# Optimization experiments

Measured on AMD Instinct MI355X. Metric: run time of the kernel, lower is better.

## Reference

```python
import jax, jax.numpy as jnp
import numpy as np

RES = 32
EPS = 1e-06


def setup_inputs() -> dict:
    key = jax.random.key(0)
    k1, k2 = jax.random.split(key)
    features = jax.random.normal(k1, (16, 32768, 64), dtype=jnp.float32)
    # coords roughly in [-1, 1] as the docstring assumes
    coords = jax.random.uniform(k2, (16, 32768, 3), dtype=jnp.float32, minval=-1.0, maxval=1.0)
    return {"features": features, "coords": coords}


def reference(features, coords):
    R = RES
    B, N, C = features.shape
    # center and normalize coords to [0, 1]
    centered = coords - coords.mean(axis=1, keepdims=True)               # [B,N,3]
    max_norm = jnp.linalg.norm(centered, axis=2, keepdims=True).max(axis=1, keepdims=True)  # [B,1,1]
    normalized_coords = centered / (max_norm * 2 + EPS) + 0.5            # [B,N,3] in [0,1]
    # voxel indices
    vi = jnp.round(normalized_coords * (R - 1)).astype(jnp.int32)        # [B,N,3]
    idx = vi[..., 0] * (R * R) + vi[..., 1] * R + vi[..., 2]             # [B,N]
    # flatten batch into segment ids: segment = b*R^3 + idx
    flat_idx = (idx + jnp.arange(B, dtype=jnp.int32)[:, None] * (R ** 3)).reshape(-1)  # [B*N]
    sums = jax.ops.segment_sum(features.reshape(B * N, C), flat_idx,
                               num_segments=B * R ** 3).reshape(B, R ** 3, C)
    counts = jax.ops.segment_sum(jnp.ones((B * N,), features.dtype), flat_idx,
                                 num_segments=B * R ** 3).reshape(B, R ** 3, 1)
    avg = sums / jnp.maximum(counts, 1.0)                                 # [B,R^3,C]
    avg_voxel_features = avg.transpose(0, 2, 1).reshape(B, C, R, R, R)
    return avg_voxel_features, normalized_coords
```

## Files before the change

kernel.cpp:

```cpp
#include <hip/hip_runtime.h>

#define NB     16
#define NPTS   32768
#define NC     64
#define RES    32
#define R3     32768
#define EPSV   1e-6f
#define SLICES 8
#define NPT    (NB * NPTS)

#define QSCALE 1048576.0f
#define QINV   (1.0f / 1048576.0f)
#define QBIAS  8388608

__global__ __launch_bounds__(256) void stats_partial_kernel(const float* __restrict__ coords,
                                                            double* __restrict__ psum) {
    const int blk = blockIdx.x;
    const int b = blk >> 3, s = blk & (SLICES - 1);
    const int cnt = NPTS / SLICES;
    const float* cb = coords + ((size_t)b * NPTS + (size_t)s * cnt) * 3;

    double sx = 0.0, sy = 0.0, sz = 0.0;
    for (int n = threadIdx.x; n < cnt; n += 256) {
        sx += (double)cb[n * 3 + 0];
        sy += (double)cb[n * 3 + 1];
        sz += (double)cb[n * 3 + 2];
    }
    __shared__ double sd[256];
    const int t = threadIdx.x;
    sd[t] = sx; __syncthreads();
    for (int o = 128; o > 0; o >>= 1) { if (t < o) sd[t] += sd[t + o]; __syncthreads(); }
    if (t == 0) psum[blk * 3 + 0] = sd[0];
    __syncthreads();
    sd[t] = sy; __syncthreads();
    for (int o = 128; o > 0; o >>= 1) { if (t < o) sd[t] += sd[t + o]; __syncthreads(); }
    if (t == 0) psum[blk * 3 + 1] = sd[0];
    __syncthreads();
    sd[t] = sz; __syncthreads();
    for (int o = 128; o > 0; o >>= 1) { if (t < o) sd[t] += sd[t + o]; __syncthreads(); }
    if (t == 0) psum[blk * 3 + 2] = sd[0];
}

__global__ __launch_bounds__(256) void maxnorm_partial_kernel(const float* __restrict__ coords,
                                                              const double* __restrict__ psum,
                                                              float* __restrict__ pmax) {
    const int blk = blockIdx.x;
    const int b = blk >> 3, s = blk & (SLICES - 1);
    const int cnt = NPTS / SLICES;

    double dx = 0.0, dy = 0.0, dz = 0.0;
    for (int i = 0; i < SLICES; i++) {
        dx += psum[(b * SLICES + i) * 3 + 0];
        dy += psum[(b * SLICES + i) * 3 + 1];
        dz += psum[(b * SLICES + i) * 3 + 2];
    }
    const float mx = (float)(dx / (double)NPTS);
    const float my = (float)(dy / (double)NPTS);
    const float mz = (float)(dz / (double)NPTS);

    const float* cb = coords + ((size_t)b * NPTS + (size_t)s * cnt) * 3;
    float mn = 0.0f;
    for (int n = threadIdx.x; n < cnt; n += 256) {
        float ax = cb[n * 3 + 0] - mx;
        float ay = cb[n * 3 + 1] - my;
        float az = cb[n * 3 + 2] - mz;
        mn = fmaxf(mn, sqrtf(ax * ax + ay * ay + az * az));
    }
    __shared__ float sf[256];
    const int t = threadIdx.x;
    sf[t] = mn; __syncthreads();
    for (int o = 128; o > 0; o >>= 1) { if (t < o) sf[t] = fmaxf(sf[t], sf[t + o]); __syncthreads(); }
    if (t == 0) pmax[blk] = sf[0];
}

__global__ __launch_bounds__(64) void stats_final_kernel(const double* __restrict__ psum,
                                                         const float* __restrict__ pmax,
                                                         float* __restrict__ stats) {
    const int b = threadIdx.x;
    if (b < NB) {
        double dx = 0.0, dy = 0.0, dz = 0.0; float m = 0.0f;
        for (int i = 0; i < SLICES; i++) {
            dx += psum[(b * SLICES + i) * 3 + 0];
            dy += psum[(b * SLICES + i) * 3 + 1];
            dz += psum[(b * SLICES + i) * 3 + 2];
            m  = fmaxf(m, pmax[b * SLICES + i]);
        }
        stats[b * 4 + 0] = (float)(dx / (double)NPTS);
        stats[b * 4 + 1] = (float)(dy / (double)NPTS);
        stats[b * 4 + 2] = (float)(dz / (double)NPTS);
        stats[b * 4 + 3] = m * 2.0f + EPSV;
    }
}

__global__ __launch_bounds__(256) void scatter_packed_kernel(const float* __restrict__ features,
                                                             const float* __restrict__ coords,
                                                             const float* __restrict__ stats,
                                                             unsigned long long* __restrict__ acc,
                                                             float* __restrict__ nc_out,
                                                             unsigned* __restrict__ counts) {
    const int tid = blockIdx.x * 256 + threadIdx.x;
    const int p   = tid >> 5;
    const int h   = tid & 31;
    const int b   = p >> 15;

    const float mx = stats[b * 4 + 0];
    const float my = stats[b * 4 + 1];
    const float mz = stats[b * 4 + 2];
    const float s  = stats[b * 4 + 3];

    const float nx = (coords[(size_t)p * 3 + 0] - mx) / s + 0.5f;
    const float ny = (coords[(size_t)p * 3 + 1] - my) / s + 0.5f;
    const float nz = (coords[(size_t)p * 3 + 2] - mz) / s + 0.5f;

    int vx = (int)rintf(nx * (float)(RES - 1));
    int vy = (int)rintf(ny * (float)(RES - 1));
    int vz = (int)rintf(nz * (float)(RES - 1));
    vx = min(max(vx, 0), RES - 1);
    vy = min(max(vy, 0), RES - 1);
    vz = min(max(vz, 0), RES - 1);
    const int vox = vx * (RES * RES) + vy * RES + vz;

    if (h < 3) {
        const float v = (h == 0) ? nx : ((h == 1) ? ny : nz);
        nc_out[(size_t)p * 3 + h] = v;
    }
    if (h == 0) atomicAdd(&counts[((size_t)b << 15) + vox], 1u);

    const float2 f2 = *(const float2*)(features + ((size_t)p << 6) + (h << 1));
    const int q0 = (int)rintf(f2.x * QSCALE);
    const int q1 = (int)rintf(f2.y * QSCALE);
    const unsigned long long pk =
        (unsigned long long)(unsigned)(q0 + QBIAS) |
        ((unsigned long long)(unsigned)(q1 + QBIAS) << 32);

    atomicAdd(&acc[(((size_t)((b << 15) + vox)) << 5) + h], pk);
}

__global__ __launch_bounds__(256) void finalize_kernel(const unsigned long long* __restrict__ acc,
                                                       const unsigned* __restrict__ counts,
                                                       float* __restrict__ out0) {
    const int bkt = blockIdx.x;
    const int b   = bkt >> 9;
    const int v0  = (bkt & 511) << 6;
    const int tid = threadIdx.x;

    __shared__ float    t[64][65];
    __shared__ float    rcs[64];
    __shared__ unsigned cnts[64];

    unsigned c = 0;
    if (tid < 64) {
        c = counts[((size_t)b << 15) + v0 + tid];
        cnts[tid] = c;
        rcs[tid]  = 1.0f / fmaxf((float)c, 1.0f);
    }
    const int any = __syncthreads_or(c != 0);

    float* o = out0 + ((size_t)b << 21) + v0;
    const int vl0 = (tid & 15) << 2;

    if (!any) {
        const float4 z = {0.0f, 0.0f, 0.0f, 0.0f};
#pragma unroll
        for (int k = 0; k < 4; k++) {
            const int ch = (tid >> 4) + (k << 4);
            *(float4*)(o + ((size_t)ch << 15) + vl0) = z;
        }
        return;
    }

    const unsigned long long* a = acc + (((size_t)((b << 15) + v0)) << 5);
#pragma unroll
    for (int i = 0; i < 8; i++) {
        const int f  = i * 256 + tid;
        const int v  = f >> 5;
        const int hh = f & 31;
        const unsigned long long u = a[f];
        const unsigned cv = cnts[v];
        const long long bias = (long long)cv * (long long)QBIAS;
        const long long q0 = (long long)(u & 0xffffffffull) - bias;
        const long long q1 = (long long)(u >> 32) - bias;
        const float rc = rcs[v] * QINV;
        t[v][2 * hh + 0] = (float)q0 * rc;
        t[v][2 * hh + 1] = (float)q1 * rc;
    }
    __syncthreads();

#pragma unroll
    for (int k = 0; k < 4; k++) {
        const int ch = (tid >> 4) + (k << 4);
        float4 v4;
        v4.x = t[vl0 + 0][ch];
        v4.y = t[vl0 + 1][ch];
        v4.z = t[vl0 + 2][ch];
        v4.w = t[vl0 + 3][ch];
        *(float4*)(o + ((size_t)ch << 15) + vl0) = v4;
    }
}

extern "C" void kernel_launch(void* const* d_in, const int* in_sizes, int n_in,
                              void* d_out, int out_size, void* d_ws, size_t ws_size,
                              hipStream_t stream) {
    const float* features = (const float*)d_in[0];
    const float* coords   = (const float*)d_in[1];

    float* out0   = (float*)d_out;
    float* nc_out = (float*)d_out + (size_t)NB * NC * R3;

    char* ws = (char*)d_ws;
    float*              stats  = (float*)ws;
    double*             psum   = (double*)(ws + 256);
    float*              pmax   = (float*)(ws + 3584);
    unsigned*           counts = (unsigned*)(ws + 4096);
    unsigned long long* acc    = (unsigned long long*)(ws + 4096 + (size_t)NB * R3 * 4);

    const size_t counts_bytes = (size_t)NB * R3 * 4;
    const size_t acc_bytes    = (size_t)NB * R3 * 32 * 8;

    hipMemsetAsync(counts, 0, counts_bytes + acc_bytes, stream);

    stats_partial_kernel<<<NB * SLICES, 256, 0, stream>>>(coords, psum);
    maxnorm_partial_kernel<<<NB * SLICES, 256, 0, stream>>>(coords, psum, pmax);
    stats_final_kernel<<<1, 64, 0, stream>>>(psum, pmax, stats);

    scatter_packed_kernel<<<(NPT * 32) / 256, 256, 0, stream>>>(features, coords, stats,
                                                                acc, nc_out, counts);

    finalize_kernel<<<NB * 512, 256, 0, stream>>>(acc, counts, out0);
}
```

Baseline: 383.3 us.

## Fuse coord stats into one kernel and remap blocks for XCD-local atomics

Three stats kernels (partial sum, partial max-norm, final combine) are merged into a single kernel with one 1024-thread block per batch, removing two launches and the workspace round trips. The scatter and finalize kernels remap blockIdx so that blocks dispatched round-robin to the same XCD handle a contiguous range of points or voxels. This is meant to keep each batch's accumulator atomics and reads within one XCD's L2. The trade-off is that the stats pass now runs on only 16 blocks, so it has less parallelism.

```diff
diff --git a/kernel.cpp b/kernel.cpp
--- a/kernel.cpp
+++ b/kernel.cpp
@@ -6,89 +6,59 @@
 #define RES    32
 #define R3     32768
 #define EPSV   1e-6f
-#define SLICES 8
 #define NPT    (NB * NPTS)
 
 #define QSCALE 1048576.0f
 #define QINV   (1.0f / 1048576.0f)
 #define QBIAS  8388608
 
-__global__ __launch_bounds__(256) void stats_partial_kernel(const float* __restrict__ coords,
-                                                            double* __restrict__ psum) {
-    const int blk = blockIdx.x;
-    const int b = blk >> 3, s = blk & (SLICES - 1);
-    const int cnt = NPTS / SLICES;
-    const float* cb = coords + ((size_t)b * NPTS + (size_t)s * cnt) * 3;
+__global__ __launch_bounds__(1024) void stats_kernel(const float* __restrict__ coords,
+                                                     float* __restrict__ stats) {
+    const int b = blockIdx.x;
+    const int t = threadIdx.x;
+    const float* cb = coords + (size_t)b * NPTS * 3;
 
     double sx = 0.0, sy = 0.0, sz = 0.0;
-    for (int n = threadIdx.x; n < cnt; n += 256) {
+    for (int n = t; n < NPTS; n += 1024) {
         sx += (double)cb[n * 3 + 0];
         sy += (double)cb[n * 3 + 1];
         sz += (double)cb[n * 3 + 2];
     }
-    __shared__ double sd[256];
-    const int t = threadIdx.x;
+
+    __shared__ double sd[1024];
+    __shared__ float  res[3];
+
     sd[t] = sx; __syncthreads();
-    for (int o = 128; o > 0; o >>= 1) { if (t < o) sd[t] += sd[t + o]; __syncthreads(); }
-    if (t == 0) psum[blk * 3 + 0] = sd[0];
+    for (int o = 512; o > 0; o >>= 1) { if (t < o) sd[t] += sd[t + o]; __syncthreads(); }
+    if (t == 0) res[0] = (float)(sd[0] / (double)NPTS);
     __syncthreads();
     sd[t] = sy; __syncthreads();
-    for (int o = 128; o > 0; o >>= 1) { if (t < o) sd[t] += sd[t + o]; __syncthreads(); }
-    if (t == 0) psum[blk * 3 + 1] = sd[0];
+    for (int o = 512; o > 0; o >>= 1) { if (t < o) sd[t] += sd[t + o]; __syncthreads(); }
+    if (t == 0) res[1] = (float)(sd[0] / (double)NPTS);
     __syncthreads();
     sd[t] = sz; __syncthreads();
-    for (int o = 128; o > 0; o >>= 1) { if (t < o) sd[t] += sd[t + o]; __syncthreads(); }
-    if (t == 0) psum[blk * 3 + 2] = sd[0];
-}
+    for (int o = 512; o > 0; o >>= 1) { if (t < o) sd[t] += sd[t + o]; __syncthreads(); }
+    if (t == 0) res[2] = (float)(sd[0] / (double)NPTS);
+    __syncthreads();
 
-__global__ __launch_bounds__(256) void maxnorm_partial_kernel(const float* __restrict__ coords,
-                                                              const double* __restrict__ psum,
-                                                              float* __restrict__ pmax) {
-    const int blk = blockIdx.x;
-    const int b = blk >> 3, s = blk & (SLICES - 1);
-    const int cnt = NPTS / SLICES;
+    const float mx = res[0], my = res[1], mz = res[2];
 
-    double dx = 0.0, dy = 0.0, dz = 0.0;
-    for (int i = 0; i < SLICES; i++) {
-        dx += psum[(b * SLICES + i) * 3 + 0];
-        dy += psum[(b * SLICES + i) * 3 + 1];
-        dz += psum[(b * SLICES + i) * 3 + 2];
+    float mn = 0.0f;
+    for (int n = t; n < NPTS; n += 1024) {
+        float dx = cb[n * 3 + 0] - mx;
+        float dy = cb[n * 3 + 1] - my;
+        float dz = cb[n * 3 + 2] - mz;
+        mn = fmaxf(mn, sqrtf(dx * dx + dy * dy + dz * dz));
     }
-    const float mx = (float)(dx / (double)NPTS);
-    const float my = (float)(dy / (double)NPTS);
-    const float mz = (float)(dz / (double)NPTS);
+    float* sf = (float*)sd;
+    sf[t] = mn; __syncthreads();
+    for (int o = 512; o > 0; o >>= 1) { if (t < o) sf[t] = fmaxf(sf[t], sf[t + o]); __syncthreads(); }
 
-    const float* cb = coords + ((size_t)b * NPTS + (size_t)s * cnt) * 3;
-    float mn = 0.0f;
-    for (int n = threadIdx.x; n < cnt; n += 256) {
-        float ax = cb[n * 3 + 0] - mx;
-        float ay = cb[n * 3 + 1] - my;
-        float az = cb[n * 3 + 2] - mz;
-        mn = fmaxf(mn, sqrtf(ax * ax + ay * ay + az * az));
-    }
-    __shared__ float sf[256];
-    const int t = threadIdx.x;
-    sf[t] = mn; __syncthreads();
-    for (int o = 128; o > 0; o >>= 1) { if (t < o) sf[t] = fmaxf(sf[t], sf[t + o]); __syncthreads(); }
-    if (t == 0) pmax[blk] = sf[0];
-}
-
-__global__ __launch_bounds__(64) void stats_final_kernel(const double* __restrict__ psum,
-                                                         const float* __restrict__ pmax,
-                                                         float* __restrict__ stats) {
-    const int b = threadIdx.x;
-    if (b < NB) {
-        double dx = 0.0, dy = 0.0, dz = 0.0; float m = 0.0f;
-        for (int i = 0; i < SLICES; i++) {
-            dx += psum[(b * SLICES + i) * 3 + 0];
-            dy += psum[(b * SLICES + i) * 3 + 1];
-            dz += psum[(b * SLICES + i) * 3 + 2];
-            m  = fmaxf(m, pmax[b * SLICES + i]);
-        }
-        stats[b * 4 + 0] = (float)(dx / (double)NPTS);
-        stats[b * 4 + 1] = (float)(dy / (double)NPTS);
-        stats[b * 4 + 2] = (float)(dz / (double)NPTS);
-        stats[b * 4 + 3] = m * 2.0f + EPSV;
+    if (t == 0) {
+        stats[b * 4 + 0] = mx;
+        stats[b * 4 + 1] = my;
+        stats[b * 4 + 2] = mz;
+        stats[b * 4 + 3] = sf[0] * 2.0f + EPSV;
     }
 }
 
@@ -98,10 +68,11 @@
                                                              unsigned long long* __restrict__ acc,
                                                              float* __restrict__ nc_out,
                                                              unsigned* __restrict__ counts) {
-    const int tid = blockIdx.x * 256 + threadIdx.x;
-    const int p   = tid >> 5;
-    const int h   = tid & 31;
-    const int b   = p >> 15;
+    const int xcd  = blockIdx.x & 7;
+    const int slot = blockIdx.x >> 3;
+    const int p    = (xcd << 16) | (slot << 3) | (threadIdx.x >> 5);
+    const int h    = threadIdx.x & 31;
+    const int b    = p >> 15;
 
     const float mx = stats[b * 4 + 0];
     const float my = stats[b * 4 + 1];
@@ -139,7 +110,7 @@
 __global__ __launch_bounds__(256) void finalize_kernel(const unsigned long long* __restrict__ acc,
                                                        const unsigned* __restrict__ counts,
                                                        float* __restrict__ out0) {
-    const int bkt = blockIdx.x;
+    const int bkt = ((blockIdx.x & 7) << 10) | (blockIdx.x >> 3);
     const int b   = bkt >> 9;
     const int v0  = (bkt & 511) << 6;
     const int tid = threadIdx.x;
@@ -176,8 +147,7 @@
         const int v  = f >> 5;
         const int hh = f & 31;
         const unsigned long long u = a[f];
-        const unsigned cv = cnts[v];
-        const long long bias = (long long)cv * (long long)QBIAS;
+        const long long bias = (long long)cnts[v] * (long long)QBIAS;
         const long long q0 = (long long)(u & 0xffffffffull) - bias;
         const long long q1 = (long long)(u >> 32) - bias;
         const float rc = rcs[v] * QINV;
@@ -209,8 +179,6 @@
 
     char* ws = (char*)d_ws;
     float*              stats  = (float*)ws;
-    double*             psum   = (double*)(ws + 256);
-    float*              pmax   = (float*)(ws + 3584);
     unsigned*           counts = (unsigned*)(ws + 4096);
     unsigned long long* acc    = (unsigned long long*)(ws + 4096 + (size_t)NB * R3 * 4);
 
@@ -219,9 +187,7 @@
 
     hipMemsetAsync(counts, 0, counts_bytes + acc_bytes, stream);
 
-    stats_partial_kernel<<<NB * SLICES, 256, 0, stream>>>(coords, psum);
-    maxnorm_partial_kernel<<<NB * SLICES, 256, 0, stream>>>(coords, psum, pmax);
-    stats_final_kernel<<<1, 64, 0, stream>>>(psum, pmax, stats);
+    stats_kernel<<<NB, 1024, 0, stream>>>(coords, stats);
 
     scatter_packed_kernel<<<(NPT * 32) / 256, 256, 0, stream>>>(features, coords, stats,
                                                                 acc, nc_out, counts);
```

Result: no change. 378.6 us (-1.2%).
